# Performance work log

Hardware: AMD Instinct MI355X
Metric: run time of the kernel (lower is better)

Reference implementation:

```python
import jax, jax.numpy as jnp
import numpy as np

N = 100000        # nodes
E = 1600000       # edges (avg degree 16)
D = 128           # feature dim (in_dim == out_dim)
L = 3             # num_layers
P = 8             # num_parts


def setup_inputs() -> dict:
    key = jax.random.key(0)
    k1, k2, k3, k4, k5, k6 = jax.random.split(key, 6)
    edge_row = jnp.sort(jax.random.randint(k1, (E,), 0, N))
    edge_col = jax.random.randint(k2, (E,), 0, N)
    edge_vals = jax.random.uniform(k3, (E,), dtype=jnp.float32)
    x = jax.random.normal(k4, (N, D), dtype=jnp.float32)
    stacked_params = jax.random.normal(k5, (L, D, D, P), dtype=jnp.float32)
    layer_weights = jax.random.normal(k6, (L, P), dtype=jnp.float32)
    return {"edge_row": edge_row, "edge_col": edge_col, "edge_vals": edge_vals,
            "x": x, "stacked_params": stacked_params, "layer_weights": layer_weights}


def reference(edge_row, edge_col, edge_vals, x, stacked_params, layer_weights):
    n = x.shape[0]
    num_layers = stacked_params.shape[0]
    h = x
    for i in range(num_layers):
        # sparse adj.spmm(h): gather source features, scale by edge value, sum per row
        msg = h[edge_col] * edge_vals[:, None]                       # [E, D]
        ax = jax.ops.segment_sum(msg, edge_row, num_segments=n)      # [N, D]
        # MyLinear: softmax over the num_parts weight, contract parts dim
        w = jax.nn.softmax(layer_weights[i])                         # [P]
        ww = jnp.einsum('oip,p->oi', stacked_params[i], w)           # [D_out, D_in]
        h = ax @ ww.T                                                # [N, D_out]
        if i < num_layers - 1:
            h = jax.nn.relu(h)
    return h
```

## Files before the change

kernel.cpp:

```cpp
#include <hip/hip_runtime.h>
#include <cstdint>

#define D 128
#define P 8
#define L 3

typedef __attribute__((ext_vector_type(8))) _Float16 f16x8;
typedef __attribute__((ext_vector_type(4))) float    f32x4;
typedef __attribute__((ext_vector_type(2))) float    f32x2;

#if __has_builtin(__builtin_amdgcn_cvt_pk_f32_fp8) && __has_builtin(__builtin_amdgcn_cvt_pk_fp8_f32)
#define HAVE_FP8_CVT 1
#else
#define HAVE_FP8_CVT 0
#endif

static __device__ __forceinline__ f32x2 fp8x2_to_f32(uint32_t u) {
#if HAVE_FP8_CVT
    return __builtin_amdgcn_cvt_pk_f32_fp8((int)u, false);
#else
    f32x2 r;
#pragma unroll
    for (int i = 0; i < 2; i++) {
        uint32_t b = (u >> (8 * i)) & 0xffu;
        uint32_t mag = b & 0x7fu;
        uint16_t h = (uint16_t)(((b & 0x80u) << 8) | ((mag >= 8u) ? ((mag << 7) + 0x2000u) : 0u));
        union { uint16_t q; _Float16 hf; } c; c.q = h;
        r[i] = (float)c.hf;
    }
    return r;
#endif
}

static __device__ __forceinline__ uint32_t f32_to_fp8(float v) {
#if HAVE_FP8_CVT
    return (uint32_t)__builtin_amdgcn_cvt_pk_fp8_f32(v, v, 0, false) & 0xffu;
#else
    union { _Float16 hf; uint16_t q; } c; c.hf = (_Float16)v;
    uint32_t s = ((uint32_t)c.q >> 8) & 0x80u;
    int t = (int)(c.q & 0x7fff) - 0x2000;
    if (t < 0) return s;
    int r = (t + 63 + ((t >> 7) & 1)) >> 7;
    if (r > 0x7e) r = 0x7e;
    return s | (uint32_t)r;
#endif
}

__global__ void prep_edges(const int* __restrict__ er, const int* __restrict__ col,
                           const float* __restrict__ vals,
                           int* __restrict__ rp, uint32_t* __restrict__ epk,
                           int n, int e) {
    int i = blockIdx.x * blockDim.x + threadIdx.x;
    if (i >= e) return;
    union { _Float16 h; uint16_t u; } v;
    v.h = (_Float16)vals[i];
    epk[i] = ((uint32_t)col[i] << 15) | (uint32_t)(v.u & 0x7FFFu);

    int cur = er[i];
    if (i == 0) {
        for (int r = 0; r <= cur; r++) rp[r] = 0;
    } else {
        int prev = er[i - 1];
        for (int r = prev + 1; r <= cur; r++) rp[r] = i;
    }
    if (i == e - 1) {
        for (int r = cur + 1; r <= n; r++) rp[r] = e;
    }
}

__global__ void build_ww(const float* __restrict__ sp, const float* __restrict__ lw,
                         _Float16* __restrict__ wwB) {
    int idx = blockIdx.x * blockDim.x + threadIdx.x;
    if (idx >= L * D * D) return;
    int l = idx / (D * D);
    int rem = idx - l * D * D;
    int o = rem / D;
    int i = rem - o * D;
    float wv[P];
    float m = -1e30f;
#pragma unroll
    for (int p = 0; p < P; p++) { wv[p] = lw[l * P + p]; m = fmaxf(m, wv[p]); }
    float s = 0.f;
#pragma unroll
    for (int p = 0; p < P; p++) { wv[p] = __expf(wv[p] - m); s += wv[p]; }
    float inv = 1.0f / s;
    const float* spp = sp + ((size_t)(l * D + o) * D + i) * P;
    float acc = 0.f;
#pragma unroll
    for (int p = 0; p < P; p++) acc += spp[p] * wv[p];
    int kt = i >> 5, kp = i & 31;
    wwB[(((l * 4 + kt) * D + o) << 5) + kp] = (_Float16)(acc * inv);
}

static __device__ __forceinline__ void mfma_store16_q8(const _Float16 (*s_h)[136],
                                                       const _Float16* __restrict__ wwB_l,
                                                       uint8_t* __restrict__ y8,
                                                       float* __restrict__ scl,
                                                       unsigned* srow,
                                                       int row0, int n, int tid) {
    const int w = tid >> 6, lane = tid & 63;
    const int quad = lane >> 4, l16 = lane & 15;
    f32x4 acc[2] = {};
#pragma unroll
    for (int kt = 0; kt < 4; kt++) {
        f16x8 af = *(const f16x8*)&s_h[l16][kt * 32 + quad * 8];
#pragma unroll
        for (int c = 0; c < 2; c++) {
            const int ct = w * 2 + c;
            f16x8 bf = *(const f16x8*)&wwB_l[((kt * D + ct * 16 + l16) << 5) + quad * 8];
            acc[c] = __builtin_amdgcn_mfma_f32_16x16x32_f16(af, bf, acc[c], 0, 0, 0);
        }
    }
#pragma unroll
    for (int rg = 0; rg < 4; rg++) {
        float m = fmaxf(fabsf(acc[0][rg]), fabsf(acc[1][rg]));
#pragma unroll
        for (int d = 1; d < 16; d <<= 1) m = fmaxf(m, __shfl_xor(m, d));
        if (l16 == 0) atomicMax(&srow[quad * 4 + rg], __float_as_uint(m));
    }
    __syncthreads();
#pragma unroll
    for (int rg = 0; rg < 4; rg++) {
        const int rr = quad * 4 + rg;
        const int row = row0 + rr;
        float rmax = fmaxf(__uint_as_float(srow[rr]), 1e-20f);
        float qs = 448.f / rmax;
        if (row < n) {
#pragma unroll
            for (int c = 0; c < 2; c++) {
                const int ct = w * 2 + c;
                float v = acc[c][rg] * qs;
                v = fminf(fmaxf(v, -448.f), 448.f);
                y8[row * D + ct * 16 + l16] = (uint8_t)f32_to_fp8(v);
            }
            if (w == 0 && l16 == 0) scl[row] = rmax * (1.f / 448.f);
        }
    }
}

__global__ __launch_bounds__(256, 8)
void gemm_x32(const float* __restrict__ x, const _Float16* __restrict__ wwB_l,
              uint8_t* __restrict__ y8, float* __restrict__ scl, int n) {
    __shared__ _Float16 s_h[16][136];
    __shared__ unsigned srow[16];
    const int tid = threadIdx.x;
    const int row0 = blockIdx.x * 16;
    const int c8 = (tid & 15) * 8;
    if (tid < 16) srow[tid] = 0;
    {
        int r = tid >> 4;
        int row = row0 + r;
        float4 v0 = {}, v1 = {};
        if (row < n) {
            v0 = *(const float4*)&x[row * D + c8];
            v1 = *(const float4*)&x[row * D + c8 + 4];
        }
        f16x8 h;
        h[0] = (_Float16)v0.x; h[1] = (_Float16)v0.y;
        h[2] = (_Float16)v0.z; h[3] = (_Float16)v0.w;
        h[4] = (_Float16)v1.x; h[5] = (_Float16)v1.y;
        h[6] = (_Float16)v1.z; h[7] = (_Float16)v1.w;
        *(f16x8*)&s_h[r][c8] = h;
    }
    __syncthreads();
    mfma_store16_q8(s_h, wwB_l, y8, scl, srow, row0, n, tid);
}

template<int NB>
static __device__ __forceinline__ void gather_chunk(float& a0, float& a1,
                                                    const uint8_t* __restrict__ y8,
                                                    const uint32_t* __restrict__ epk,
                                                    const float* __restrict__ scl,
                                                    int e, int l2) {
    uint32_t m[NB];
#pragma unroll
    for (int j = 0; j < NB; j++) m[j] = epk[e + j];
    float sc[NB];
#pragma unroll
    for (int j = 0; j < NB; j++) sc[j] = scl[m[j] >> 15];
    uint32_t g[NB];
#pragma unroll
    for (int j = 0; j < NB; j++)
        g[j] = *(const uint16_t*)&y8[(m[j] >> 15) * (uint32_t)D + (uint32_t)l2];
#pragma unroll
    for (int j = 0; j < NB; j++) {
        union { uint16_t u; _Float16 h; } vv; vv.u = (uint16_t)(m[j] & 0x7FFFu);
        float vf = (float)vv.h * sc[j];
        f32x2 p = fp8x2_to_f32(g[j]);
        a0 += vf * p[0];
        a1 += vf * p[1];
    }
}

static __device__ __forceinline__ void gather_row64(float& a0, float& a1,
                                                    const uint8_t* __restrict__ y8,
                                                    const uint32_t* __restrict__ epk,
                                                    const float* __restrict__ scl,
                                                    int e, int e1, int l2) {
    for (; e + 16 <= e1; e += 16) gather_chunk<16>(a0, a1, y8, epk, scl, e, l2);
    if (e + 8 <= e1) { gather_chunk<8>(a0, a1, y8, epk, scl, e, l2); e += 8; }
    if (e + 4 <= e1) { gather_chunk<4>(a0, a1, y8, epk, scl, e, l2); e += 4; }
    for (; e < e1; e++) gather_chunk<1>(a0, a1, y8, epk, scl, e, l2);
}

__global__ __launch_bounds__(256, 8)
void fused_layer(const uint8_t* __restrict__ yprev, const float* __restrict__ sprev,
                 const int* __restrict__ rp, const uint32_t* __restrict__ epk,
                 const _Float16* __restrict__ wwB_l,
                 uint8_t* __restrict__ ynext, float* __restrict__ snext, int n) {
    __shared__ _Float16 s_h[16][136];
    __shared__ unsigned srow[16];
    const int tid = threadIdx.x;
    const int lane = tid & 63;
    const int l2 = lane * 2;
    const int w = __builtin_amdgcn_readfirstlane(tid >> 6);
    const int row0 = blockIdx.x * 16;
    const int rbase = row0 + w * 4;
    if (tid < 16) srow[tid] = 0;
#pragma unroll 1
    for (int q = 0; q < 4; q++) {
        const int r = rbase + q;
        float a0 = 0.f, a1 = 0.f;
        if (r < n) {
            int e  = __builtin_amdgcn_readfirstlane(rp[r]);
            int e1 = __builtin_amdgcn_readfirstlane(rp[r + 1]);
            gather_row64(a0, a1, yprev, epk, sprev, e, e1, l2);
        }
        union { uint32_t u; _Float16 h[2]; } o;
        o.h[0] = (_Float16)fmaxf(a0, 0.f);
        o.h[1] = (_Float16)fmaxf(a1, 0.f);
        *(uint32_t*)&s_h[w * 4 + q][l2] = o.u;
    }
    __syncthreads();
    mfma_store16_q8(s_h, wwB_l, ynext, snext, srow, row0, n, tid);
}

__global__ __launch_bounds__(256, 8)
void spmm_f32(const uint8_t* __restrict__ y8, const float* __restrict__ sprev,
              const int* __restrict__ rp, const uint32_t* __restrict__ epk,
              float* __restrict__ out, int n) {
    const int tid = threadIdx.x;
    const int lane = tid & 63;
    const int l2 = lane * 2;
    const int w = __builtin_amdgcn_readfirstlane(tid >> 6);
    const int rbase = blockIdx.x * 16 + w * 4;
#pragma unroll 1
    for (int q = 0; q < 4; q++) {
        const int r = rbase + q;
        if (r >= n) continue;
        float a0 = 0.f, a1 = 0.f;
        int e  = __builtin_amdgcn_readfirstlane(rp[r]);
        int e1 = __builtin_amdgcn_readfirstlane(rp[r + 1]);
        gather_row64(a0, a1, y8, epk, sprev, e, e1, l2);
        *(float2*)&out[(size_t)r * D + l2] = make_float2(a0, a1);
    }
}

extern "C" void kernel_launch(void* const* d_in, const int* in_sizes, int n_in,
                              void* d_out, int out_size, void* d_ws, size_t ws_size,
                              hipStream_t stream) {
    const int*   edge_row  = (const int*)d_in[0];
    const int*   edge_col  = (const int*)d_in[1];
    const float* edge_vals = (const float*)d_in[2];
    const float* x         = (const float*)d_in[3];
    const float* sp        = (const float*)d_in[4];
    const float* lw        = (const float*)d_in[5];
    float* out = (float*)d_out;

    const int E_ = in_sizes[0];
    const int N_ = in_sizes[3] / D;

    char* ws = (char*)d_ws;
    int* row_ptr = (int*)ws;
    size_t off = (((size_t)(N_ + 1) * sizeof(int)) + 255) & ~(size_t)255;
    uint32_t* epk = (uint32_t*)(ws + off);
    off += (size_t)E_ * sizeof(uint32_t);
    off = (off + 255) & ~(size_t)255;
    _Float16* wwB = (_Float16*)(ws + off);
    off += (size_t)L * 4 * D * 32 * sizeof(_Float16);
    off = (off + 255) & ~(size_t)255;
    uint8_t* y8A = (uint8_t*)(ws + off);
    off += (size_t)N_ * D;
    uint8_t* y8B = (uint8_t*)(ws + off);
    off += (size_t)N_ * D;
    off = (off + 255) & ~(size_t)255;
    float* scA = (float*)(ws + off);
    off += (size_t)N_ * sizeof(float);
    float* scB = (float*)(ws + off);

    prep_edges<<<(E_ + 255) / 256, 256, 0, stream>>>(edge_row, edge_col, edge_vals,
                                                     row_ptr, epk, N_, E_);
    build_ww<<<(L * D * D + 255) / 256, 256, 0, stream>>>(sp, lw, wwB);

    const int sblk = (N_ + 15) / 16;
    const int WWL = 4 * D * 32;

    gemm_x32<<<sblk, 256, 0, stream>>>(x, wwB, y8A, scA, N_);
    fused_layer<<<sblk, 256, 0, stream>>>(y8A, scA, row_ptr, epk, wwB + WWL,     y8B, scB, N_);
    fused_layer<<<sblk, 256, 0, stream>>>(y8B, scB, row_ptr, epk, wwB + 2 * WWL, y8A, scA, N_);
    spmm_f32<<<sblk, 256, 0, stream>>>(y8A, scA, row_ptr, epk, out, N_);
}
```

Baseline: 295.9 us.

## Map 16 lanes per row with 8-byte fp8 gathers in SpMM kernels

The sparse gather is remapped from one wavefront per row (each lane loading 2 fp8 bytes, 4 rows in sequence) to 16 threads per row, each loading 8 fp8 bytes and keeping 8 accumulators, so all 16 rows of a block are gathered at once. This widens each memory access and raises the number of rows in flight, cutting per-row serialization and load-instruction count. Row bounds are no longer wave-uniform, because four rows share a wavefront and diverge on degree. More registers are needed, so launch bounds drop from 8 to 6 blocks per CU.

Result: faster. 266.7 us (-9.9%).

```diff
diff --git a/kernel.cpp b/kernel.cpp
--- a/kernel.cpp
+++ b/kernel.cpp
@@ -15,14 +15,16 @@
 #define HAVE_FP8_CVT 0
 #endif
 
-static __device__ __forceinline__ f32x2 fp8x2_to_f32(uint32_t u) {
+template<bool HI>
+static __device__ __forceinline__ f32x2 fp8_pair(uint32_t u) {
 #if HAVE_FP8_CVT
-    return __builtin_amdgcn_cvt_pk_f32_fp8((int)u, false);
+    return __builtin_amdgcn_cvt_pk_f32_fp8((int)u, HI);
 #else
+    uint32_t w = HI ? (u >> 16) : u;
     f32x2 r;
 #pragma unroll
     for (int i = 0; i < 2; i++) {
-        uint32_t b = (u >> (8 * i)) & 0xffu;
+        uint32_t b = (w >> (8 * i)) & 0xffu;
         uint32_t mag = b & 0x7fu;
         uint16_t h = (uint16_t)(((b & 0x80u) << 8) | ((mag >= 8u) ? ((mag << 7) + 0x2000u) : 0u));
         union { uint16_t q; _Float16 hf; } c; c.q = h;
@@ -167,43 +169,44 @@
 }
 
 template<int NB>
-static __device__ __forceinline__ void gather_chunk(float& a0, float& a1,
-                                                    const uint8_t* __restrict__ y8,
-                                                    const uint32_t* __restrict__ epk,
-                                                    const float* __restrict__ scl,
-                                                    int e, int l2) {
+static __device__ __forceinline__ void gather_chunk8(float (&a)[8],
+                                                     const uint8_t* __restrict__ y8,
+                                                     const uint32_t* __restrict__ epk,
+                                                     const float* __restrict__ scl,
+                                                     int e, int c8) {
     uint32_t m[NB];
 #pragma unroll
     for (int j = 0; j < NB; j++) m[j] = epk[e + j];
-    float sc[NB];
-#pragma unroll
-    for (int j = 0; j < NB; j++) sc[j] = scl[m[j] >> 15];
-    uint32_t g[NB];
-#pragma unroll
-    for (int j = 0; j < NB; j++)
-        g[j] = *(const uint16_t*)&y8[(m[j] >> 15) * (uint32_t)D + (uint32_t)l2];
+    uint2 g[NB]; float sc[NB];
+#pragma unroll
+    for (int j = 0; j < NB; j++) {
+        uint32_t row = m[j] >> 15;
+        g[j]  = *(const uint2*)&y8[row * (uint32_t)D + (uint32_t)c8];
+        sc[j] = scl[row];
+    }
 #pragma unroll
     for (int j = 0; j < NB; j++) {
         union { uint16_t u; _Float16 h; } vv; vv.u = (uint16_t)(m[j] & 0x7FFFu);
         float vf = (float)vv.h * sc[j];
-        f32x2 p = fp8x2_to_f32(g[j]);
-        a0 += vf * p[0];
-        a1 += vf * p[1];
-    }
-}
-
-static __device__ __forceinline__ void gather_row64(float& a0, float& a1,
-                                                    const uint8_t* __restrict__ y8,
-                                                    const uint32_t* __restrict__ epk,
-                                                    const float* __restrict__ scl,
-                                                    int e, int e1, int l2) {
-    for (; e + 16 <= e1; e += 16) gather_chunk<16>(a0, a1, y8, epk, scl, e, l2);
-    if (e + 8 <= e1) { gather_chunk<8>(a0, a1, y8, epk, scl, e, l2); e += 8; }
-    if (e + 4 <= e1) { gather_chunk<4>(a0, a1, y8, epk, scl, e, l2); e += 4; }
-    for (; e < e1; e++) gather_chunk<1>(a0, a1, y8, epk, scl, e, l2);
-}
-
-__global__ __launch_bounds__(256, 8)
+        f32x2 p;
+        p = fp8_pair<false>(g[j].x); a[0] += vf * p[0]; a[1] += vf * p[1];
+        p = fp8_pair<true >(g[j].x); a[2] += vf * p[0]; a[3] += vf * p[1];
+        p = fp8_pair<false>(g[j].y); a[4] += vf * p[0]; a[5] += vf * p[1];
+        p = fp8_pair<true >(g[j].y); a[6] += vf * p[0]; a[7] += vf * p[1];
+    }
+}
+
+static __device__ __forceinline__ void gather_row8(float (&a)[8],
+                                                   const uint8_t* __restrict__ y8,
+                                                   const uint32_t* __restrict__ epk,
+                                                   const float* __restrict__ scl,
+                                                   int e, int e1, int c8) {
+    for (; e + 8 <= e1; e += 8) gather_chunk8<8>(a, y8, epk, scl, e, c8);
+    if (e + 4 <= e1) { gather_chunk8<4>(a, y8, epk, scl, e, c8); e += 4; }
+    for (; e < e1; e++) gather_chunk8<1>(a, y8, epk, scl, e, c8);
+}
+
+__global__ __launch_bounds__(256, 6)
 void fused_layer(const uint8_t* __restrict__ yprev, const float* __restrict__ sprev,
                  const int* __restrict__ rp, const uint32_t* __restrict__ epk,
                  const _Float16* __restrict__ wwB_l,
@@ -211,49 +214,35 @@
     __shared__ _Float16 s_h[16][136];
     __shared__ unsigned srow[16];
     const int tid = threadIdx.x;
-    const int lane = tid & 63;
-    const int l2 = lane * 2;
-    const int w = __builtin_amdgcn_readfirstlane(tid >> 6);
     const int row0 = blockIdx.x * 16;
-    const int rbase = row0 + w * 4;
+    const int sg = tid >> 4;
+    const int c8 = (tid & 15) * 8;
     if (tid < 16) srow[tid] = 0;
-#pragma unroll 1
-    for (int q = 0; q < 4; q++) {
-        const int r = rbase + q;
-        float a0 = 0.f, a1 = 0.f;
-        if (r < n) {
-            int e  = __builtin_amdgcn_readfirstlane(rp[r]);
-            int e1 = __builtin_amdgcn_readfirstlane(rp[r + 1]);
-            gather_row64(a0, a1, yprev, epk, sprev, e, e1, l2);
-        }
-        union { uint32_t u; _Float16 h[2]; } o;
-        o.h[0] = (_Float16)fmaxf(a0, 0.f);
-        o.h[1] = (_Float16)fmaxf(a1, 0.f);
-        *(uint32_t*)&s_h[w * 4 + q][l2] = o.u;
+    {
+        int r = row0 + sg;
+        float a[8] = {0.f, 0.f, 0.f, 0.f, 0.f, 0.f, 0.f, 0.f};
+        if (r < n) gather_row8(a, yprev, epk, sprev, rp[r], rp[r + 1], c8);
+        f16x8 o;
+#pragma unroll
+        for (int k = 0; k < 8; k++) o[k] = (_Float16)fmaxf(a[k], 0.f);
+        *(f16x8*)&s_h[sg][c8] = o;
     }
     __syncthreads();
     mfma_store16_q8(s_h, wwB_l, ynext, snext, srow, row0, n, tid);
 }
 
-__global__ __launch_bounds__(256, 8)
+__global__ __launch_bounds__(256, 6)
 void spmm_f32(const uint8_t* __restrict__ y8, const float* __restrict__ sprev,
               const int* __restrict__ rp, const uint32_t* __restrict__ epk,
               float* __restrict__ out, int n) {
     const int tid = threadIdx.x;
-    const int lane = tid & 63;
-    const int l2 = lane * 2;
-    const int w = __builtin_amdgcn_readfirstlane(tid >> 6);
-    const int rbase = blockIdx.x * 16 + w * 4;
-#pragma unroll 1
-    for (int q = 0; q < 4; q++) {
-        const int r = rbase + q;
-        if (r >= n) continue;
-        float a0 = 0.f, a1 = 0.f;
-        int e  = __builtin_amdgcn_readfirstlane(rp[r]);
-        int e1 = __builtin_amdgcn_readfirstlane(rp[r + 1]);
-        gather_row64(a0, a1, y8, epk, sprev, e, e1, l2);
-        *(float2*)&out[(size_t)r * D + l2] = make_float2(a0, a1);
-    }
+    const int r = blockIdx.x * 16 + (tid >> 4);
+    const int c8 = (tid & 15) * 8;
+    if (r >= n) return;
+    float a[8] = {0.f, 0.f, 0.f, 0.f, 0.f, 0.f, 0.f, 0.f};
+    gather_row8(a, y8, epk, sprev, rp[r], rp[r + 1], c8);
+    *(float4*)&out[(size_t)r * D + c8]     = make_float4(a[0], a[1], a[2], a[3]);
+    *(float4*)&out[(size_t)r * D + c8 + 4] = make_float4(a[4], a[5], a[6], a[7]);
 }
 
 extern "C" void kernel_launch(void* const* d_in, const int* in_sizes, int n_in,
```
